# Kernel tuning notes

Hardware: AMD Instinct MI355X
Metric: run time of the kernel (lower is better)

The kernel has to match this reference:

```python
import jax, jax.numpy as jnp
import numpy as np

N_NODES = 100000


def gcn_conv(x, edge_index, edge_weight, W, b):
    """PyG GCNConv: out = D^-1/2 (A + I) D^-1/2 X W + b (self-loop weight 1)."""
    n = x.shape[0]
    src, dst = edge_index[0], edge_index[1]
    loop = jnp.arange(n)
    src_sl = jnp.concatenate([src, loop])
    dst_sl = jnp.concatenate([dst, loop])
    ew_sl = jnp.concatenate([edge_weight, jnp.ones((n,), x.dtype)])
    deg = jax.ops.segment_sum(ew_sl, dst_sl, num_segments=n)  # [N]
    dinv = jnp.where(deg > 0, jax.lax.rsqrt(deg), 0.0)
    norm = dinv[src_sl] * ew_sl * dinv[dst_sl]  # [E+N]
    h = x @ W  # [N, out_dim] dense transform before propagation
    msg = h[src_sl] * norm[:, None]  # gather + scale, [E+N, out_dim]
    out = jax.ops.segment_sum(msg, dst_sl, num_segments=n)  # scatter-add
    return out + b


def setup_inputs() -> dict:
    key = jax.random.key(0)
    ks = jax.random.split(key, 9)
    in_dim, hidden, latent = 128, 64, 32
    n, e = N_NODES, 1600000
    x = jax.random.normal(ks[0], (n, in_dim), dtype=jnp.float32)
    edge_index = jax.random.randint(ks[1], (2, e), 0, n, dtype=jnp.int64)
    edge_weight = jax.random.uniform(ks[2], (e,), dtype=jnp.float32)
    def glorot(k, fan_in, fan_out):
        s = jnp.sqrt(6.0 / (fan_in + fan_out))
        return jax.random.uniform(k, (fan_in, fan_out), jnp.float32, -s, s)
    return {
        "x": x,
        "edge_index": edge_index,
        "edge_weight": edge_weight,
        "W1": glorot(ks[3], in_dim, hidden),
        "b1": jnp.zeros((hidden,), jnp.float32),
        "W_mu": glorot(ks[4], hidden, latent),
        "b_mu": jnp.zeros((latent,), jnp.float32),
        "W_lv": glorot(ks[5], hidden, latent),
        "b_lv": jnp.zeros((latent,), jnp.float32),
    }


def reference(x, edge_index, edge_weight, W1, b1, W_mu, b_mu, W_lv, b_lv):
    h = jax.nn.relu(gcn_conv(x, edge_index, edge_weight, W1, b1))
    mu = gcn_conv(h, edge_index, edge_weight, W_mu, b_mu)
    logvar = gcn_conv(h, edge_index, edge_weight, W_lv, b_lv)
    return (mu, logvar)
```

## Files before the change

kernel.cpp:

```cpp
#include <hip/hip_runtime.h>

static __device__ __forceinline__ float4 ld4(const float* p) { return *(const float4*)p; }
static __device__ __forceinline__ float b2f(unsigned short u) {
    return __uint_as_float((unsigned)u << 16);
}
static __device__ __forceinline__ float b2f_lo(unsigned u) { return __uint_as_float(u << 16); }
static __device__ __forceinline__ float b2f_hi(unsigned u) { return __uint_as_float(u & 0xFFFF0000u); }
static __device__ __forceinline__ unsigned short f2b(float f) {
    unsigned x = __float_as_uint(f);
    return (unsigned short)((x + 0x7FFFu + ((x >> 16) & 1u)) >> 16);
}
static __device__ __forceinline__ unsigned pk2(float lo, float hi) {
    return (unsigned)f2b(lo) | ((unsigned)f2b(hi) << 16);
}

typedef __attribute__((ext_vector_type(8))) short bf16x8;
typedef __attribute__((ext_vector_type(4))) float f32x4;

#define NPB 256
#define CAPE 5120



__global__ __launch_bounds__(256) void k_fused1(const float* __restrict__ A,
                                                const float* __restrict__ W0,
                                                unsigned short* __restrict__ gout,
                                                const int* __restrict__ src,
                                                const int* __restrict__ dst,
                                                const float* __restrict__ ew,
                                                int* __restrict__ bin_cnt,
                                                unsigned long long* __restrict__ ebuf,
                                                int n, int E, int gb, int NB) {
    __shared__ unsigned short xh[64 * 136];
    __shared__ unsigned short xl[64 * 136];
    __shared__ unsigned short Wth[64 * 136];
    __shared__ unsigned short Wtl[64 * 136];
    __shared__ int hist[512];
    __shared__ int hbase[512];
    int tid = threadIdx.x;

    if ((int)blockIdx.x < gb) {
        int row0 = blockIdx.x * 64;
        for (int j = tid; j < 2048; j += 256) {
            int c = j >> 5, kq = (j & 31) * 4;
            ushort4 uh, ul;
            #pragma unroll
            for (int i = 0; i < 4; i++) {
                float wv = W0[(size_t)(kq + i) * 64 + c];
                unsigned short hi = f2b(wv);
                unsigned short lo = f2b(wv - b2f(hi));
                ((unsigned short*)&uh)[i] = hi;
                ((unsigned short*)&ul)[i] = lo;
            }
            *(ushort4*)&Wth[c * 136 + kq] = uh;
            *(ushort4*)&Wtl[c * 136 + kq] = ul;
        }
        for (int j = tid; j < 2048; j += 256) {
            int r = j >> 5, kc = (j & 31) * 4;
            int grow = row0 + r;
            float4 v = make_float4(0.f, 0.f, 0.f, 0.f);
            if (grow < n) v = ld4(A + (size_t)grow * 128 + kc);
            ushort4 uh, ul;
            uh.x = f2b(v.x); ul.x = f2b(v.x - b2f(uh.x));
            uh.y = f2b(v.y); ul.y = f2b(v.y - b2f(uh.y));
            uh.z = f2b(v.z); ul.z = f2b(v.z - b2f(uh.z));
            uh.w = f2b(v.w); ul.w = f2b(v.w - b2f(uh.w));
            *(ushort4*)&xh[r * 136 + kc] = uh;
            *(ushort4*)&xl[r * 136 + kc] = ul;
        }
        __syncthreads();
        int w = tid >> 6, lane = tid & 63;
        int rA = lane & 15;
        int g8 = (lane >> 4) * 8;
        f32x4 acc[4] = {{0.f, 0.f, 0.f, 0.f}, {0.f, 0.f, 0.f, 0.f},
                        {0.f, 0.f, 0.f, 0.f}, {0.f, 0.f, 0.f, 0.f}};
        #pragma unroll
        for (int kb = 0; kb < 4; kb++) {
            bf16x8 ah = *(const bf16x8*)&xh[(w * 16 + rA) * 136 + kb * 32 + g8];
            bf16x8 al = *(const bf16x8*)&xl[(w * 16 + rA) * 136 + kb * 32 + g8];
            #pragma unroll
            for (int ct = 0; ct < 4; ct++) {
                bf16x8 bh = *(const bf16x8*)&Wth[(ct * 16 + rA) * 136 + kb * 32 + g8];
                bf16x8 bl = *(const bf16x8*)&Wtl[(ct * 16 + rA) * 136 + kb * 32 + g8];
                acc[ct] = __builtin_amdgcn_mfma_f32_16x16x32_bf16(ah, bh, acc[ct], 0, 0, 0);
                acc[ct] = __builtin_amdgcn_mfma_f32_16x16x32_bf16(al, bh, acc[ct], 0, 0, 0);
                acc[ct] = __builtin_amdgcn_mfma_f32_16x16x32_bf16(ah, bl, acc[ct], 0, 0, 0);
            }
        }
        int rbase = row0 + w * 16 + (lane >> 4) * 4;
        #pragma unroll
        for (int reg = 0; reg < 4; reg++) {
            int grow = rbase + reg;
            if (grow < n) {
                #pragma unroll
                for (int ct = 0; ct < 4; ct++)
                    gout[(size_t)grow * 64 + ct * 16 + rA] = f2b(acc[ct][reg]);
            }
        }
    } else {
        for (int j = tid; j < NB; j += 256) hist[j] = 0;
        __syncthreads();
        int e0 = ((int)blockIdx.x - gb) * 4096;
        unsigned long long pk[16]; int bb[16]; int loc[16];
        #pragma unroll
        for (int j = 0; j < 16; j++) {
            int e = e0 + j * 256 + tid;
            if (e < E) {
                int s = src[e];
                int d = dst[e];
                float w = ew[e];
                bb[j] = d >> 8;
                pk[j] = ((unsigned long long)__float_as_uint(w) << 32) |
                        (unsigned)((d & (NPB - 1)) << 17) | (unsigned)s;
                loc[j] = atomicAdd(&hist[bb[j]], 1);
            } else bb[j] = -1;
        }
        __syncthreads();
        for (int j = tid; j < NB; j += 256) hbase[j] = atomicAdd(&bin_cnt[j], hist[j]);
        __syncthreads();
        #pragma unroll
        for (int j = 0; j < 16; j++) {
            if (bb[j] >= 0)
                ebuf[(size_t)bb[j] * CAPE + hbase[bb[j]] + loc[j]] = pk[j];
        }
    }
}

__global__ __launch_bounds__(512) void k_csr_build(const unsigned long long* __restrict__ ebuf,
                                                   const int* __restrict__ bin_cnt,
                                                   int2* __restrict__ rowcnt,
                                                   float* __restrict__ dinv,
                                                   unsigned long long* __restrict__ csr,
                                                   unsigned short* __restrict__ h0,
                                                   int n) {
    __shared__ unsigned long long eL[CAPE];
    __shared__ unsigned cntL[NPB];
    __shared__ unsigned ewsL[NPB];
    __shared__ unsigned fillL[NPB];
    __shared__ int scanL[512];
    __shared__ int rowL[NPB];
    __shared__ float dinvL[NPB];
    __shared__ int binbase_s;
    int b = blockIdx.x;
    int tid = threadIdx.x;
    if (tid < NPB) { cntL[tid] = 0; ewsL[tid] = 0; fillL[tid] = 0; }
    scanL[tid] = (tid < b) ? bin_cnt[tid] : 0;
    __syncthreads();
    int m = bin_cnt[b];
    const unsigned long long* eb = ebuf + (size_t)b * CAPE;
    for (int i = tid; i < m; i += 512) {
        unsigned long long pk = eb[i];
        eL[i] = pk;
        int ld = (int)((pk >> 17) & (NPB - 1));
        float w = __uint_as_float((unsigned)(pk >> 32));
        atomicAdd(&cntL[ld], 1u);
        atomicAdd(&ewsL[ld], (unsigned)(w * 16777216.0f));
    }
    __syncthreads();
    #pragma unroll
    for (int off = 256; off > 0; off >>= 1) {
        if (tid < off) scanL[tid] += scanL[tid + off];
        __syncthreads();
    }
    if (tid == 0) binbase_s = scanL[0];
    __syncthreads();
    int v = (tid < NPB) ? (int)cntL[tid] : 0;
    scanL[tid] = v;
    __syncthreads();
    #pragma unroll
    for (int off = 1; off < 512; off <<= 1) {
        int t = (tid >= off) ? scanL[tid - off] : 0;
        __syncthreads();
        scanL[tid] += t;
        __syncthreads();
    }
    if (tid < NPB) {
        int rp = binbase_s + scanL[tid] - v;
        rowL[tid] = rp;
        float dv = rsqrtf(1.0f + (float)ewsL[tid] * (1.0f / 16777216.0f));
        dinvL[tid] = dv;
        int node = b * NPB + tid;
        if (node < n) {
            rowcnt[node] = make_int2(rp, v);
            dinv[node] = dv;
        }
    }
    __syncthreads();
    for (int i = tid; i < m; i += 512) {
        unsigned long long pk = eL[i];
        int s = (int)(pk & 0x1FFFF);
        int ld = (int)((pk >> 17) & (NPB - 1));
        int pos = rowL[ld] + (int)atomicAdd(&fillL[ld], 1u);
        csr[pos] = (unsigned long long)(unsigned)s | (pk & 0xFFFFFFFF00000000ull);
    }
    for (int idx = tid; idx < NPB * 8; idx += 512) {
        int ln = idx >> 3;
        int node = b * NPB + ln;
        if (node < n) {
            float sc = dinvL[ln];
            unsigned short* hp = h0 + (size_t)node * 64 + (idx & 7) * 8;
            uint4 u = *(uint4*)hp;
            u.x = pk2(b2f_lo(u.x) * sc, b2f_hi(u.x) * sc);
            u.y = pk2(b2f_lo(u.y) * sc, b2f_hi(u.y) * sc);
            u.z = pk2(b2f_lo(u.z) * sc, b2f_hi(u.z) * sc);
            u.w = pk2(b2f_lo(u.w) * sc, b2f_hi(u.w) * sc);
            *(uint4*)hp = u;
        }
    }
}

__global__ __launch_bounds__(256) void k_gemm2(const unsigned short* __restrict__ h,
                                               const float* __restrict__ Wmu,
                                               const float* __restrict__ Wlv,
                                               const float* __restrict__ dinv,
                                               unsigned short* __restrict__ out, int n) {
    __shared__ unsigned short hA[64 * 72];
    __shared__ unsigned short Wth[64 * 72];
    __shared__ unsigned short Wtl[64 * 72];
    int tid = threadIdx.x;
    int row0 = blockIdx.x * 64;
    for (int j = tid; j < 1024; j += 256) {
        int c = j >> 4, kq = (j & 15) * 4;
        const float* Wsrc = (c < 32) ? Wmu : Wlv;
        int cc = c & 31;
        ushort4 uh, ul;
        #pragma unroll
        for (int i = 0; i < 4; i++) {
            float wv = Wsrc[(size_t)(kq + i) * 32 + cc];
            unsigned short hi = f2b(wv);
            unsigned short lo = f2b(wv - b2f(hi));
            ((unsigned short*)&uh)[i] = hi;
            ((unsigned short*)&ul)[i] = lo;
        }
        *(ushort4*)&Wth[c * 72 + kq] = uh;
        *(ushort4*)&Wtl[c * 72 + kq] = ul;
    }
    for (int j = tid; j < 512; j += 256) {
        int r = j >> 3, q = (j & 7) * 8;
        int grow = row0 + r;
        uint4 u = make_uint4(0u, 0u, 0u, 0u);
        if (grow < n) u = *(const uint4*)(h + (size_t)grow * 64 + q);
        *(uint4*)&hA[r * 72 + q] = u;
    }
    __syncthreads();
    int w = tid >> 6, lane = tid & 63;
    int rA = lane & 15;
    int g8 = (lane >> 4) * 8;
    f32x4 acc[4] = {{0.f, 0.f, 0.f, 0.f}, {0.f, 0.f, 0.f, 0.f},
                    {0.f, 0.f, 0.f, 0.f}, {0.f, 0.f, 0.f, 0.f}};
    #pragma unroll
    for (int kb = 0; kb < 2; kb++) {
        bf16x8 a = *(const bf16x8*)&hA[(w * 16 + rA) * 72 + kb * 32 + g8];
        #pragma unroll
        for (int ct = 0; ct < 4; ct++) {
            bf16x8 bh = *(const bf16x8*)&Wth[(ct * 16 + rA) * 72 + kb * 32 + g8];
            bf16x8 bl = *(const bf16x8*)&Wtl[(ct * 16 + rA) * 72 + kb * 32 + g8];
            acc[ct] = __builtin_amdgcn_mfma_f32_16x16x32_bf16(a, bh, acc[ct], 0, 0, 0);
            acc[ct] = __builtin_amdgcn_mfma_f32_16x16x32_bf16(a, bl, acc[ct], 0, 0, 0);
        }
    }
    int rbase = row0 + w * 16 + (lane >> 4) * 4;
    #pragma unroll
    for (int reg = 0; reg < 4; reg++) {
        int grow = rbase + reg;
        if (grow < n) {
            float sc = dinv[grow];
            #pragma unroll
            for (int ct = 0; ct < 4; ct++)
                out[(size_t)grow * 64 + ct * 16 + rA] = f2b(acc[ct][reg] * sc);
        }
    }
}

static __device__ __forceinline__ void acc8(float* a, uint4 r, float wt) {
    a[0] = fmaf(b2f_lo(r.x), wt, a[0]); a[1] = fmaf(b2f_hi(r.x), wt, a[1]);
    a[2] = fmaf(b2f_lo(r.y), wt, a[2]); a[3] = fmaf(b2f_hi(r.y), wt, a[3]);
    a[4] = fmaf(b2f_lo(r.z), wt, a[4]); a[5] = fmaf(b2f_hi(r.z), wt, a[5]);
    a[6] = fmaf(b2f_lo(r.w), wt, a[6]); a[7] = fmaf(b2f_hi(r.w), wt, a[7]);
}

template<bool RELU, bool SPLIT_OUT>
__global__ __launch_bounds__(256) void k_prop(const unsigned short* __restrict__ g,
                                              const int2* __restrict__ csr,
                                              const int2* __restrict__ rowcnt,
                                              const float* __restrict__ dinv,
                                              const float* __restrict__ bias0,
                                              const float* __restrict__ bias1,
                                              void* __restrict__ outv, int n) {
    int node = blockIdx.x * 4 + (threadIdx.x >> 6);
    if (node >= n) return;
    int lane = threadIdx.x & 63;
    int q = lane >> 3;
    int t = lane & 7;
    uint4 sr = *(const uint4*)(g + (size_t)node * 64 + t * 8);
    int2 rc = rowcnt[node];
    const int2* ep = csr + rc.x;
    int m = rc.y;
    float a[8] = {};
    for (int e = 0; e < m; e += 32) {
        int e1 = e + q, e2 = e1 + 8, e3 = e1 + 16, e4 = e1 + 24;
        int i1 = min(e1, m - 1), i2 = min(e2, m - 1);
        int i3 = min(e3, m - 1), i4 = min(e4, m - 1);
        int2 p1 = ep[i1];
        int2 p2 = ep[i2];
        int2 p3 = ep[i3];
        int2 p4 = ep[i4];
        uint4 r1 = *(const uint4*)(g + (size_t)p1.x * 64 + t * 8);
        uint4 r2 = *(const uint4*)(g + (size_t)p2.x * 64 + t * 8);
        uint4 r3 = *(const uint4*)(g + (size_t)p3.x * 64 + t * 8);
        uint4 r4 = *(const uint4*)(g + (size_t)p4.x * 64 + t * 8);
        float w1 = (e1 < m) ? __int_as_float(p1.y) : 0.f;
        float w2 = (e2 < m) ? __int_as_float(p2.y) : 0.f;
        float w3 = (e3 < m) ? __int_as_float(p3.y) : 0.f;
        float w4 = (e4 < m) ? __int_as_float(p4.y) : 0.f;
        acc8(a, r1, w1);
        acc8(a, r2, w2);
        acc8(a, r3, w3);
        acc8(a, r4, w4);
    }
    #pragma unroll
    for (int i = 0; i < 8; i++) {
        a[i] += __shfl_xor(a[i], 8);
        a[i] += __shfl_xor(a[i], 16);
        a[i] += __shfl_xor(a[i], 32);
    }
    if (q != 0) return;
    a[0] += b2f_lo(sr.x); a[1] += b2f_hi(sr.x);
    a[2] += b2f_lo(sr.y); a[3] += b2f_hi(sr.y);
    a[4] += b2f_lo(sr.z); a[5] += b2f_hi(sr.z);
    a[6] += b2f_lo(sr.w); a[7] += b2f_hi(sr.w);
    float di = dinv[node];
    #pragma unroll
    for (int i = 0; i < 8; i++) a[i] *= di;
    if (!SPLIT_OUT) {
        float4 b0 = ld4(bias0 + t * 8);
        float4 b1 = ld4(bias0 + t * 8 + 4);
        a[0] += b0.x; a[1] += b0.y; a[2] += b0.z; a[3] += b0.w;
        a[4] += b1.x; a[5] += b1.y; a[6] += b1.z; a[7] += b1.w;
        if (RELU) {
            #pragma unroll
            for (int i = 0; i < 8; i++) a[i] = fmaxf(a[i], 0.f);
        }
        uint4 u = make_uint4(pk2(a[0], a[1]), pk2(a[2], a[3]),
                             pk2(a[4], a[5]), pk2(a[6], a[7]));
        *(uint4*)((unsigned short*)outv + (size_t)node * 64 + t * 8) = u;
    } else {
        float* out = (float*)outv;
        const float* bp = (t < 4) ? (bias0 + t * 8) : (bias1 + (t - 4) * 8);
        size_t base = (t < 4) ? ((size_t)node * 32 + t * 8)
                              : ((size_t)n * 32 + (size_t)node * 32 + (t - 4) * 8);
        float4 b0 = ld4(bp);
        float4 b1 = ld4(bp + 4);
        float4 v0 = make_float4(a[0] + b0.x, a[1] + b0.y, a[2] + b0.z, a[3] + b0.w);
        float4 v1 = make_float4(a[4] + b1.x, a[5] + b1.y, a[6] + b1.z, a[7] + b1.w);
        *(float4*)&out[base] = v0;
        *(float4*)&out[base + 4] = v1;
    }
}

extern "C" void kernel_launch(void* const* d_in, const int* in_sizes, int n_in,
                              void* d_out, int out_size, void* d_ws, size_t ws_size,
                              hipStream_t stream) {
    const float* x   = (const float*)d_in[0];
    const int*   ei  = (const int*)d_in[1];
    const float* ew  = (const float*)d_in[2];
    const float* W1  = (const float*)d_in[3];
    const float* b1  = (const float*)d_in[4];
    const float* Wmu = (const float*)d_in[5];
    const float* bmu = (const float*)d_in[6];
    const float* Wlv = (const float*)d_in[7];
    const float* blv = (const float*)d_in[8];
    float* outp = (float*)d_out;

    const int n = in_sizes[0] / 128;
    const int E = in_sizes[2];
    const int* src = ei;
    const int* dst = ei + E;
    const int NB = (n + NPB - 1) / NPB;

    size_t o = 0;
    auto alloc = [&](size_t bytes) { void* p = (char*)d_ws + o; o += (bytes + 511) & ~(size_t)511; return p; };
    int*   bin_cnt  = (int*)alloc((size_t)NB * 4);
    int2*  rowcnt   = (int2*)alloc((size_t)n * 8);
    float* dinv     = (float*)alloc((size_t)n * 4);
    unsigned long long* csr  = (unsigned long long*)alloc((size_t)E * 8);
    unsigned long long* ebuf = (unsigned long long*)alloc((size_t)NB * CAPE * 8);
    unsigned short* g0 = (unsigned short*)alloc((size_t)n * 64 * 2);
    unsigned short* h  = (unsigned short*)alloc((size_t)n * 64 * 2);
    unsigned short* g2 = g0;

    const int gb = (n + 63) / 64;
    const int bb = (E + 4095) / 4096;

    hipMemsetAsync(bin_cnt, 0, (size_t)NB * 4, stream);
    k_fused1<<<gb + bb, 256, 0, stream>>>(x, W1, g0, src, dst, ew,
                                          bin_cnt, ebuf, n, E, gb, NB);
    k_csr_build<<<NB, 512, 0, stream>>>(ebuf, bin_cnt, rowcnt, dinv, csr, g0, n);
    k_prop<true, false><<<(n + 3) / 4, 256, 0, stream>>>(g0, (const int2*)csr, rowcnt, dinv,
                                                         b1, nullptr, h, n);
    k_gemm2<<<gb, 256, 0, stream>>>(h, Wmu, Wlv, dinv, g2, n);
    k_prop<false, true><<<(n + 3) / 4, 256, 0, stream>>>(g2, (const int2*)csr, rowcnt, dinv,
                                                         bmu, blv, outp, n);
}
```

Measured before the change: 288.8 us.

## Prepack weights into MFMA fragment layout and load GEMM operands directly from global

Adds a small prep kernel that splits W1 and the concatenated Wmu/Wlv into bf16 hi/lo pairs, stored in the per-lane MFMA fragment order. Both GEMM kernels then drop their shared-memory staging and barrier. Each lane reads its x or h row slice and the packed weight fragments straight from global memory, and splits x into hi/lo by truncation rather than rounding. This removes the per-block weight conversion and LDS traffic and lowers LDS use in the fused kernel, which may raise occupancy. In exchange it adds a kernel launch, uses uncoalesced per-lane row loads, and slightly changes the x split rounding.

```diff
diff --git a/kernel.cpp b/kernel.cpp
--- a/kernel.cpp
+++ b/kernel.cpp
@@ -22,8 +22,55 @@
 
 
 
+__global__ __launch_bounds__(256) void k_prep(const float* __restrict__ W1,
+                                              const float* __restrict__ Wmu,
+                                              const float* __restrict__ Wlv,
+                                              unsigned short* __restrict__ Wf1,
+                                              unsigned short* __restrict__ Wf2) {
+    int tid = threadIdx.x;
+    if (blockIdx.x == 0) {
+        for (int idx = tid; idx < 2048; idx += 256) {
+            int frag = idx >> 6, lane = idx & 63;
+            int s = frag & 1, ct = (frag >> 1) & 3, kb = frag >> 3;
+            int rA = lane & 15, g8 = (lane >> 4) * 8;
+            int c = ct * 16 + rA;
+            unsigned short* dstp = Wf1 + frag * 512 + lane * 8;
+            for (int j = 0; j < 8; j++) {
+                float wv = W1[(size_t)(kb * 32 + g8 + j) * 64 + c];
+                unsigned short hi = f2b(wv);
+                dstp[j] = (s == 0) ? hi : f2b(wv - b2f(hi));
+            }
+        }
+    } else {
+        for (int idx = tid; idx < 1024; idx += 256) {
+            int frag = idx >> 6, lane = idx & 63;
+            int s = frag & 1, ct = (frag >> 1) & 3, kb = frag >> 3;
+            int rA = lane & 15, g8 = (lane >> 4) * 8;
+            int c = ct * 16 + rA;
+            int k0 = kb * 32 + g8;
+            unsigned short* dstp = Wf2 + frag * 512 + lane * 8;
+            for (int j = 0; j < 8; j++) {
+                float wv = (c < 32) ? Wmu[(size_t)(k0 + j) * 32 + c]
+                                    : Wlv[(size_t)(k0 + j) * 32 + (c - 32)];
+                unsigned short hi = f2b(wv);
+                dstp[j] = (s == 0) ? hi : f2b(wv - b2f(hi));
+            }
+        }
+    }
+}
+
+static __device__ __forceinline__ void split8(const float* xv, bf16x8& ah, bf16x8& al) {
+    #pragma unroll
+    for (int j = 0; j < 8; j++) {
+        unsigned u = __float_as_uint(xv[j]);
+        float res = xv[j] - __uint_as_float(u & 0xFFFF0000u);
+        ah[j] = (short)(u >> 16);
+        al[j] = (short)(__float_as_uint(res) >> 16);
+    }
+}
+
 __global__ __launch_bounds__(256) void k_fused1(const float* __restrict__ A,
-                                                const float* __restrict__ W0,
+                                                const unsigned short* __restrict__ Wf1,
                                                 unsigned short* __restrict__ gout,
                                                 const int* __restrict__ src,
                                                 const int* __restrict__ dst,
@@ -31,57 +78,30 @@
                                                 int* __restrict__ bin_cnt,
                                                 unsigned long long* __restrict__ ebuf,
                                                 int n, int E, int gb, int NB) {
-    __shared__ unsigned short xh[64 * 136];
-    __shared__ unsigned short xl[64 * 136];
-    __shared__ unsigned short Wth[64 * 136];
-    __shared__ unsigned short Wtl[64 * 136];
     __shared__ int hist[512];
     __shared__ int hbase[512];
     int tid = threadIdx.x;
 
     if ((int)blockIdx.x < gb) {
         int row0 = blockIdx.x * 64;
-        for (int j = tid; j < 2048; j += 256) {
-            int c = j >> 5, kq = (j & 31) * 4;
-            ushort4 uh, ul;
-            #pragma unroll
-            for (int i = 0; i < 4; i++) {
-                float wv = W0[(size_t)(kq + i) * 64 + c];
-                unsigned short hi = f2b(wv);
-                unsigned short lo = f2b(wv - b2f(hi));
-                ((unsigned short*)&uh)[i] = hi;
-                ((unsigned short*)&ul)[i] = lo;
-            }
-            *(ushort4*)&Wth[c * 136 + kq] = uh;
-            *(ushort4*)&Wtl[c * 136 + kq] = ul;
-        }
-        for (int j = tid; j < 2048; j += 256) {
-            int r = j >> 5, kc = (j & 31) * 4;
-            int grow = row0 + r;
-            float4 v = make_float4(0.f, 0.f, 0.f, 0.f);
-            if (grow < n) v = ld4(A + (size_t)grow * 128 + kc);
-            ushort4 uh, ul;
-            uh.x = f2b(v.x); ul.x = f2b(v.x - b2f(uh.x));
-            uh.y = f2b(v.y); ul.y = f2b(v.y - b2f(uh.y));
-            uh.z = f2b(v.z); ul.z = f2b(v.z - b2f(uh.z));
-            uh.w = f2b(v.w); ul.w = f2b(v.w - b2f(uh.w));
-            *(ushort4*)&xh[r * 136 + kc] = uh;
-            *(ushort4*)&xl[r * 136 + kc] = ul;
-        }
-        __syncthreads();
         int w = tid >> 6, lane = tid & 63;
-        int rA = lane & 15;
-        int g8 = (lane >> 4) * 8;
+        int rA = lane & 15, g8 = (lane >> 4) * 8;
+        int row = row0 + w * 16 + rA;
+        const float* xr = A + (size_t)min(row, n - 1) * 128;
         f32x4 acc[4] = {{0.f, 0.f, 0.f, 0.f}, {0.f, 0.f, 0.f, 0.f},
                         {0.f, 0.f, 0.f, 0.f}, {0.f, 0.f, 0.f, 0.f}};
         #pragma unroll
         for (int kb = 0; kb < 4; kb++) {
-            bf16x8 ah = *(const bf16x8*)&xh[(w * 16 + rA) * 136 + kb * 32 + g8];
-            bf16x8 al = *(const bf16x8*)&xl[(w * 16 + rA) * 136 + kb * 32 + g8];
+            float4 v0 = ld4(xr + kb * 32 + g8);
+            float4 v1 = ld4(xr + kb * 32 + g8 + 4);
+            float xv[8] = {v0.x, v0.y, v0.z, v0.w, v1.x, v1.y, v1.z, v1.w};
+            bf16x8 ah, al;
+            split8(xv, ah, al);
+            const unsigned short* wb = Wf1 + (size_t)(kb * 8) * 512 + lane * 8;
             #pragma unroll
             for (int ct = 0; ct < 4; ct++) {
-                bf16x8 bh = *(const bf16x8*)&Wth[(ct * 16 + rA) * 136 + kb * 32 + g8];
-                bf16x8 bl = *(const bf16x8*)&Wtl[(ct * 16 + rA) * 136 + kb * 32 + g8];
+                bf16x8 bh = *(const bf16x8*)(wb + (ct * 2 + 0) * 512);
+                bf16x8 bl = *(const bf16x8*)(wb + (ct * 2 + 1) * 512);
                 acc[ct] = __builtin_amdgcn_mfma_f32_16x16x32_bf16(ah, bh, acc[ct], 0, 0, 0);
                 acc[ct] = __builtin_amdgcn_mfma_f32_16x16x32_bf16(al, bh, acc[ct], 0, 0, 0);
                 acc[ct] = __builtin_amdgcn_mfma_f32_16x16x32_bf16(ah, bl, acc[ct], 0, 0, 0);
@@ -210,51 +230,25 @@
 }
 
 __global__ __launch_bounds__(256) void k_gemm2(const unsigned short* __restrict__ h,
-                                               const float* __restrict__ Wmu,
-                                               const float* __restrict__ Wlv,
+                                               const unsigned short* __restrict__ Wf2,
                                                const float* __restrict__ dinv,
                                                unsigned short* __restrict__ out, int n) {
-    __shared__ unsigned short hA[64 * 72];
-    __shared__ unsigned short Wth[64 * 72];
-    __shared__ unsigned short Wtl[64 * 72];
     int tid = threadIdx.x;
     int row0 = blockIdx.x * 64;
-    for (int j = tid; j < 1024; j += 256) {
-        int c = j >> 4, kq = (j & 15) * 4;
-        const float* Wsrc = (c < 32) ? Wmu : Wlv;
-        int cc = c & 31;
-        ushort4 uh, ul;
-        #pragma unroll
-        for (int i = 0; i < 4; i++) {
-            float wv = Wsrc[(size_t)(kq + i) * 32 + cc];
-            unsigned short hi = f2b(wv);
-            unsigned short lo = f2b(wv - b2f(hi));
-            ((unsigned short*)&uh)[i] = hi;
-            ((unsigned short*)&ul)[i] = lo;
-        }
-        *(ushort4*)&Wth[c * 72 + kq] = uh;
-        *(ushort4*)&Wtl[c * 72 + kq] = ul;
-    }
-    for (int j = tid; j < 512; j += 256) {
-        int r = j >> 3, q = (j & 7) * 8;
-        int grow = row0 + r;
-        uint4 u = make_uint4(0u, 0u, 0u, 0u);
-        if (grow < n) u = *(const uint4*)(h + (size_t)grow * 64 + q);
-        *(uint4*)&hA[r * 72 + q] = u;
-    }
-    __syncthreads();
     int w = tid >> 6, lane = tid & 63;
-    int rA = lane & 15;
-    int g8 = (lane >> 4) * 8;
+    int rA = lane & 15, g8 = (lane >> 4) * 8;
+    int row = row0 + w * 16 + rA;
+    const unsigned short* hr = h + (size_t)min(row, n - 1) * 64;
     f32x4 acc[4] = {{0.f, 0.f, 0.f, 0.f}, {0.f, 0.f, 0.f, 0.f},
                     {0.f, 0.f, 0.f, 0.f}, {0.f, 0.f, 0.f, 0.f}};
     #pragma unroll
     for (int kb = 0; kb < 2; kb++) {
-        bf16x8 a = *(const bf16x8*)&hA[(w * 16 + rA) * 72 + kb * 32 + g8];
+        bf16x8 a = *(const bf16x8*)(hr + kb * 32 + g8);
+        const unsigned short* wb = Wf2 + (size_t)(kb * 8) * 512 + lane * 8;
         #pragma unroll
         for (int ct = 0; ct < 4; ct++) {
-            bf16x8 bh = *(const bf16x8*)&Wth[(ct * 16 + rA) * 72 + kb * 32 + g8];
-            bf16x8 bl = *(const bf16x8*)&Wtl[(ct * 16 + rA) * 72 + kb * 32 + g8];
+            bf16x8 bh = *(const bf16x8*)(wb + (ct * 2 + 0) * 512);
+            bf16x8 bl = *(const bf16x8*)(wb + (ct * 2 + 1) * 512);
             acc[ct] = __builtin_amdgcn_mfma_f32_16x16x32_bf16(a, bh, acc[ct], 0, 0, 0);
             acc[ct] = __builtin_amdgcn_mfma_f32_16x16x32_bf16(a, bl, acc[ct], 0, 0, 0);
         }
@@ -387,18 +381,21 @@
     unsigned long long* ebuf = (unsigned long long*)alloc((size_t)NB * CAPE * 8);
     unsigned short* g0 = (unsigned short*)alloc((size_t)n * 64 * 2);
     unsigned short* h  = (unsigned short*)alloc((size_t)n * 64 * 2);
+    unsigned short* Wf1 = (unsigned short*)alloc(32 * 512 * 2);
+    unsigned short* Wf2 = (unsigned short*)alloc(16 * 512 * 2);
     unsigned short* g2 = g0;
 
     const int gb = (n + 63) / 64;
     const int bb = (E + 4095) / 4096;
 
+    k_prep<<<2, 256, 0, stream>>>(W1, Wmu, Wlv, Wf1, Wf2);
     hipMemsetAsync(bin_cnt, 0, (size_t)NB * 4, stream);
-    k_fused1<<<gb + bb, 256, 0, stream>>>(x, W1, g0, src, dst, ew,
+    k_fused1<<<gb + bb, 256, 0, stream>>>(x, Wf1, g0, src, dst, ew,
                                           bin_cnt, ebuf, n, E, gb, NB);
     k_csr_build<<<NB, 512, 0, stream>>>(ebuf, bin_cnt, rowcnt, dinv, csr, g0, n);
     k_prop<true, false><<<(n + 3) / 4, 256, 0, stream>>>(g0, (const int2*)csr, rowcnt, dinv,
                                                          b1, nullptr, h, n);
-    k_gemm2<<<gb, 256, 0, stream>>>(h, Wmu, Wlv, dinv, g2, n);
+    k_gemm2<<<gb, 256, 0, stream>>>(h, Wf2, dinv, g2, n);
     k_prop<false, true><<<(n + 3) / 4, 256, 0, stream>>>(g2, (const int2*)csr, rowcnt, dinv,
                                                          bmu, blv, outp, n);
 }
```

After: 278.3 us. 3.7% less time.
